# Performance work log

Hardware: AMD Instinct MI355X
Metric: run time of the kernel (lower is better)

Reference implementation:

```python
import jax, jax.numpy as jnp
import numpy as np

NE = 256          # number of electrons
D = 256           # attention_dim = num_heads * heads_dim
H = 4             # num_heads
DH = 64           # heads_dim
L = 2             # num_layers
NDETS = 1
MASK_LEN = 0.1


def _ln(x, s, b):
    m = jnp.mean(x, -1, keepdims=True)
    v = jnp.var(x, -1, keepdims=True)
    return (x - m) * jax.lax.rsqrt(v + 1e-5) * s + b


def setup_inputs() -> dict:
    key = jax.random.key(0)
    ks = jax.random.split(key, 16)
    n = lambda k, sh, sc: (jax.random.normal(k, sh) * sc).astype(jnp.float32)
    theta = jax.random.uniform(ks[0], (NE,), minval=0.1, maxval=np.pi - 0.1)
    phi = jax.random.uniform(ks[1], (NE,), minval=0.0, maxval=2.0 * np.pi)
    return {
        "electrons": jnp.stack([theta, phi], -1).astype(jnp.float32),
        "W_in": n(ks[2], (3, D), 3 ** -0.5),
        "Wq": n(ks[3], (L, D, H, DH), D ** -0.5),
        "bq": jnp.zeros((L, H, DH), jnp.float32),
        "Wk": n(ks[4], (L, D, H, DH), D ** -0.5),
        "bk": jnp.zeros((L, H, DH), jnp.float32),
        "Wv": n(ks[5], (L, D, H, DH), D ** -0.5),
        "bv": jnp.zeros((L, H, DH), jnp.float32),
        "Wo": n(ks[6], (L, H, DH, D), D ** -0.5),
        "bo": jnp.zeros((L, D), jnp.float32),
        "W1": n(ks[7], (L, D, D), D ** -0.5),
        "ln1_s": jnp.ones((L, D), jnp.float32),
        "ln1_b": jnp.zeros((L, D), jnp.float32),
        "W2": n(ks[8], (L, D, D), D ** -0.5),
        "b2": jnp.zeros((L, D), jnp.float32),
        "ln2_s": jnp.ones((L, D), jnp.float32),
        "ln2_b": jnp.zeros((L, D), jnp.float32),
        "Worb_r": n(ks[9], (D, NDETS * 2), D ** -0.5),
        "Worb_i": n(ks[10], (D, NDETS * 2), D ** -0.5),
    }


def reference(electrons, W_in, Wq, bq, Wk, bk, Wv, bv, Wo, bo, W1, ln1_s, ln1_b,
              W2, b2, ln2_s, ln2_b, Worb_r, Worb_i):
    theta, phi = electrons[..., 0], electrons[..., 1]
    # ---- pair gather: P = NE*(NE-1)/2 unordered pairs ----
    iu, ju = jnp.triu_indices(NE, k=1)
    th_p = jnp.stack([theta[iu], theta[ju]], -1)   # [P, 2]
    ph_p = jnp.stack([phi[iu], phi[ju]], -1)       # [P, 2]
    # input_feature: (cos t, sin t cos p, sin t sin p)
    feat = jnp.stack([jnp.cos(th_p), jnp.sin(th_p) * jnp.cos(ph_p),
                      jnp.sin(th_p) * jnp.sin(ph_p)], -1)  # [P, 2, 3]
    # ---- batched mini-transformer over all pairs (seq len 2) ----
    h = feat @ W_in  # [P, 2, D]
    for l in range(L):
        q = jnp.einsum('psd,dhk->pshk', h, Wq[l]) + bq[l]
        k = jnp.einsum('psd,dhk->pshk', h, Wk[l]) + bk[l]
        v = jnp.einsum('psd,dhk->pshk', h, Wv[l]) + bv[l]
        logits = jnp.einsum('pshk,pthk->phst', q / np.sqrt(DH), k)
        attn = jax.nn.softmax(logits, axis=-1)
        o = jnp.einsum('phst,pthk->pshk', attn, v)
        mha = jnp.einsum('pshk,hkd->psd', o, Wo[l]) + bo[l]
        h = h + mha @ W1[l]
        h = _ln(h, ln1_s[l], ln1_b[l])
        h = h + jnp.tanh(h @ W2[l] + b2[l])
        h = _ln(h, ln2_s[l], ln2_b[l])
    # ---- pair orbitals: complex dense -> [P, ndets, 2 elec, 2 orb] ----
    orb = (h @ Worb_r + 1j * (h @ Worb_i)).astype(jnp.complex64)  # [P, 2, ndets*2]
    orb = orb.reshape(-1, 2, NDETS, 2).transpose(0, 2, 1, 3)      # [P, ndets, 2, 2]
    # ---- pairwise truncation factor ----
    u = jnp.cos(th_p / 2) * jnp.exp(1j * ph_p / 2)   # [P, 2]
    v_ = jnp.sin(th_p / 2) * jnp.exp(-1j * ph_p / 2)
    chord = jnp.abs(u[:, 0] * v_[:, 1] - u[:, 1] * v_[:, 0])
    trunc = 1.0 - jnp.exp(-(chord / MASK_LEN) ** 2)  # [P]
    orb = orb * trunc[:, None, None, None]
    dets = jnp.linalg.det(orb)          # [P, ndets]
    pair_orbs = jnp.sum(dets, axis=-1)  # [P]
    # ---- scatter into antisymmetric NE x NE matrix ----
    pf = jnp.zeros((NE, NE), jnp.complex64).at[iu, ju].set(pair_orbs)
    pf = pf - pf.T
    # ---- cusp matrix ----
    ue = jnp.cos(theta / 2) * jnp.exp(0.5j * phi)   # [NE]
    ve = jnp.sin(theta / 2) * jnp.exp(-0.5j * phi)
    elem = ue[:, None] * ve[None, :] - ve[:, None] * ue[None, :]  # [NE, NE]
    eye = jnp.eye(NE, dtype=jnp.float32)
    elem_c = elem + eye
    rho_c = jnp.abs(elem_c)
    cusp = elem_c * jnp.exp(-(rho_c / MASK_LEN) ** 2)
    # ---- pfaffian = sqrt(det), in log space for stability ----
    sign, logabs = jnp.linalg.slogdet(pf + cusp)
    log_ferm = 0.5 * (logabs.astype(jnp.complex64) + 1j * jnp.angle(sign))
    # ---- bosonic flux attachment (truncated product), in log space ----
    rho = jnp.abs(elem)
    masked = jnp.sqrt(MASK_LEN ** 2 + rho ** 2) * elem / (rho + eye) + eye
    log_bos = jnp.sum(jnp.log(masked.astype(jnp.complex64)))
    return log_ferm + log_bos
```

## Files before the change

### kernel.cpp

```cpp
#include <hip/hip_runtime.h>
#include <math.h>
#include <stdint.h>

#define NE 256
#define DD 256
#define NL 2
#define P_TOT 32640
#define NB 32
#define NBP 40
#define NPANEL (NE / NB)
#define NXCD 8

typedef __bf16 bf16x8 __attribute__((ext_vector_type(8)));
typedef float f32x4 __attribute__((ext_vector_type(4)));

__device__ __forceinline__ float bf2f(ushort h) {
    union { unsigned u; float f; } c; c.u = ((unsigned)h) << 16; return c.f;
}
__device__ __forceinline__ ushort f2bf(float f) {
    union { float f; unsigned u; } c; c.f = f;
    unsigned u = c.u;
    return (ushort)((u + 0x7fffu + ((u >> 16) & 1u)) >> 16);
}

#define GLD16(gp, lp) __builtin_amdgcn_global_load_lds( \
    (const __attribute__((address_space(1))) unsigned int*)(uintptr_t)(gp), \
    (__attribute__((address_space(3))) unsigned int*)(uintptr_t)(lp), 16, 0, 0)

__global__ void idx_k(int* __restrict__ ip, int* __restrict__ jp) {
    int i = threadIdx.x;
    int base = i * 255 - (i * (i - 1)) / 2;
    for (int j = i + 1; j < NE; ++j) {
        ip[base + j - i - 1] = i;
        jp[base + j - i - 1] = j;
    }
}

__global__ void zero_k(float* __restrict__ acc) {
    if (threadIdx.x < 8) acc[threadIdx.x] = 0.f;
}

__global__ __launch_bounds__(256) void prep_w_k(
    const float* __restrict__ Wq, const float* __restrict__ Wk, const float* __restrict__ Wv,
    const float* __restrict__ Wo, const float* __restrict__ W1, const float* __restrict__ W2,
    ushort* __restrict__ Wqkv_t, ushort* __restrict__ Woth_t) {
    __shared__ float Ts[32][33];
    int z = blockIdx.z, l = z / 6, m = z % 6;
    const float* src;
    ushort* dst;
    if (m == 0)      { src = Wq + l * 65536; dst = Wqkv_t + (size_t)l * 768 * 256 + 0 * 65536; }
    else if (m == 1) { src = Wk + l * 65536; dst = Wqkv_t + (size_t)l * 768 * 256 + 1 * 65536; }
    else if (m == 2) { src = Wv + l * 65536; dst = Wqkv_t + (size_t)l * 768 * 256 + 2 * 65536; }
    else             { src = (m == 3 ? Wo : m == 4 ? W1 : W2) + l * 65536;
                       dst = Woth_t + (size_t)(l * 3 + (m - 3)) * 65536; }
    int k0 = blockIdx.x * 32, n0 = blockIdx.y * 32;
    int t = threadIdx.x, tr = t >> 5, tc = t & 31;
    for (int i = tr; i < 32; i += 8) Ts[i][tc] = src[(size_t)(k0 + i) * 256 + n0 + tc];
    __syncthreads();
    for (int i = tr; i < 32; i += 8) dst[(size_t)(n0 + i) * 256 + k0 + tc] = f2bf(Ts[tc][i]);
}

__global__ void prep_b_k(const float* __restrict__ bq, const float* __restrict__ bk,
                         const float* __restrict__ bv, float* __restrict__ bqkv) {
    int l = blockIdx.x, t = threadIdx.x;
    bqkv[l * 768 + t] = bq[l * 256 + t];
    bqkv[l * 768 + 256 + t] = bk[l * 256 + t];
    bqkv[l * 768 + 512 + t] = bv[l * 256 + t];
}

__global__ __launch_bounds__(256) void fuse_w_k(
    const float* __restrict__ Wo, const float* __restrict__ W1,
    ushort* __restrict__ Wf_t) {
    __shared__ float WoS[32][33];
    __shared__ float W1S[32][33];
    int l = blockIdx.z;
    int n0 = blockIdx.x * 32, d0 = blockIdx.y * 32;
    const float* wo = Wo + l * 65536;
    const float* w1 = W1 + l * 65536;
    int t = threadIdx.x, ty = t >> 5, tx = t & 31;
    float acc4[4] = {0.f, 0.f, 0.f, 0.f};
    for (int m0 = 0; m0 < 256; m0 += 32) {
        __syncthreads();
        for (int i = ty; i < 32; i += 8) {
            WoS[i][tx] = wo[(size_t)(d0 + i) * 256 + m0 + tx];
            W1S[i][tx] = w1[(size_t)(m0 + i) * 256 + n0 + tx];
        }
        __syncthreads();
#pragma unroll
        for (int jm = 0; jm < 32; ++jm) {
            float a = WoS[tx][jm];
#pragma unroll
            for (int q = 0; q < 4; ++q)
                acc4[q] += a * W1S[jm][ty + 8 * q];
        }
    }
#pragma unroll
    for (int q = 0; q < 4; ++q)
        Wf_t[(size_t)l * 65536 + (size_t)(n0 + ty + 8 * q) * 256 + d0 + tx] = f2bf(acc4[q]);
}

__global__ void fuse_b_k(const float* __restrict__ bo, const float* __restrict__ W1,
                         float* __restrict__ bfuse) {
    int l = blockIdx.x, n = threadIdx.x;
    const float* w1 = W1 + l * 65536;
    const float* b = bo + l * 256;
    float s = 0.f;
    for (int m = 0; m < 256; ++m) s += b[m] * w1[(size_t)m * 256 + n];
    bfuse[l * 256 + n] = s;
}

__global__ __launch_bounds__(256) void embed_k(
    const float* __restrict__ el, const float* __restrict__ Win,
    const int* __restrict__ ip, const int* __restrict__ jp,
    ushort* __restrict__ h, int P0) {
    int w = threadIdx.x >> 6, lane = threadIdx.x & 63;
    int r = blockIdx.x * 4 + w;
    int gp = P0 + (r >> 1);
    int e = (r & 1) ? jp[gp] : ip[gp];
    float th = el[2 * e], ph = el[2 * e + 1];
    float st = sinf(th);
    float f0 = cosf(th), f1 = st * cosf(ph), f2 = st * sinf(ph);
    int n = lane * 4;
    float4 w0 = *(const float4*)&Win[n];
    float4 w1 = *(const float4*)&Win[256 + n];
    float4 w2 = *(const float4*)&Win[512 + n];
    ushort4 o;
    o.x = f2bf(f0 * w0.x + f1 * w1.x + f2 * w2.x);
    o.y = f2bf(f0 * w0.y + f1 * w1.y + f2 * w2.y);
    o.z = f2bf(f0 * w0.z + f1 * w1.z + f2 * w2.z);
    o.w = f2bf(f0 * w0.w + f1 * w1.w + f2 * w2.w);
    *(ushort4*)&h[(size_t)r * 256 + n] = o;
}

template <bool BIAS, bool RES>
__global__ __launch_bounds__(256) void gemm_k(
    const ushort* __restrict__ A, int lda,
    const ushort* __restrict__ Bt,
    const float* __restrict__ bias,
    const ushort* __restrict__ Rm, int ldr,
    ushort* __restrict__ C, int ldc, int ny) {
    __shared__ ushort As[128 * 64];
    __shared__ ushort Bs[128 * 64];
    int t = threadIdx.x, lane = t & 63, w = t >> 6;
    int nwg = gridDim.x;
    int orig = blockIdx.x;
    int qq = nwg / NXCD, rr = nwg % NXCD;
    int xcd = orig % NXCD, idx = orig / NXCD;
    int wg = (xcd < rr ? xcd * (qq + 1) : rr * (qq + 1) + (xcd - rr) * qq) + idx;
    int row0 = (wg / ny) * 128, col0 = (wg % ny) * 128;
    int lrow = lane >> 3;
    int kx = ((lane & 7) ^ lrow) << 3;
    const ushort* gA = A + (size_t)(row0 + w * 32 + lrow) * lda + kx;
    const ushort* gB = Bt + (size_t)(col0 + w * 32 + lrow) * 256 + kx;
    f32x4 acc[4][4];
#pragma unroll
    for (int i = 0; i < 4; ++i)
#pragma unroll
        for (int j = 0; j < 4; ++j) acc[i][j] = (f32x4){0.f, 0.f, 0.f, 0.f};
    int wm = w >> 1, wn = w & 1;
    int mbase = wm * 64 + (lane & 15);
    int nbase = wn * 64 + (lane & 15);
    int l7 = lane & 7;
    for (int k0 = 0; k0 < 256; k0 += 64) {
        __syncthreads();
#pragma unroll
        for (int c2 = 0; c2 < 4; ++c2) {
            GLD16(gA + (size_t)(c2 * 8) * lda + k0, &As[(w * 4 + c2) * 512]);
            GLD16(gB + (size_t)(c2 * 8) * 256 + k0, &Bs[(w * 4 + c2) * 512]);
        }
        __syncthreads();
#pragma unroll
        for (int ks = 0; ks < 2; ++ks) {
            int kb = ks * 4 + (lane >> 4);
            bf16x8 af[4], bfr[4];
#pragma unroll
            for (int tm = 0; tm < 4; ++tm)
                af[tm] = *(const bf16x8*)&As[(mbase + tm * 16) * 64 + ((kb ^ l7) << 3)];
#pragma unroll
            for (int tn = 0; tn < 4; ++tn)
                bfr[tn] = *(const bf16x8*)&Bs[(nbase + tn * 16) * 64 + ((kb ^ l7) << 3)];
#pragma unroll
            for (int tm = 0; tm < 4; ++tm)
#pragma unroll
                for (int tn = 0; tn < 4; ++tn)
                    acc[tm][tn] = __builtin_amdgcn_mfma_f32_16x16x32_bf16(
                        af[tm], bfr[tn], acc[tm][tn], 0, 0, 0);
        }
    }
    int q = lane >> 4;
    int crow = row0 + wm * 64 + q * 4;
    int ccol = col0 + wn * 64 + (lane & 15);
#pragma unroll
    for (int tm = 0; tm < 4; ++tm)
#pragma unroll
        for (int r = 0; r < 4; ++r) {
            int row = crow + tm * 16 + r;
#pragma unroll
            for (int tn = 0; tn < 4; ++tn) {
                int col = ccol + tn * 16;
                float v = acc[tm][tn][r];
                if (BIAS) v += bias[col];
                if (RES) v += bf2f(Rm[(size_t)row * ldr + col]);
                C[(size_t)row * ldc + col] = f2bf(v);
            }
        }
}

template <bool TANH>
__global__ __launch_bounds__(512) void gemm_ln_k(
    const ushort* __restrict__ A, int lda,
    const ushort* __restrict__ Bt,
    const float* __restrict__ bias,
    const ushort* __restrict__ Rm,
    const float* __restrict__ sc, const float* __restrict__ bi,
    ushort* __restrict__ C) {
    __shared__ ushort As[128 * 64];
    __shared__ ushort Bs[256 * 64];
    __shared__ float red_s[128][4][2];
    int t = threadIdx.x, lane = t & 63, w = t >> 6;
    int row0 = blockIdx.x * 128;
    int lrow = lane >> 3;
    int kx = ((lane & 7) ^ lrow) << 3;
    const ushort* gA = A + (size_t)(row0 + w * 16 + lrow) * lda + kx;
    const ushort* gB = Bt + (size_t)(w * 32 + lrow) * 256 + kx;
    f32x4 acc[4][4];
#pragma unroll
    for (int i = 0; i < 4; ++i)
#pragma unroll
        for (int j = 0; j < 4; ++j) acc[i][j] = (f32x4){0.f, 0.f, 0.f, 0.f};
    int wm = w >> 2, wn = w & 3;
    int mbase = wm * 64 + (lane & 15);
    int nbase = wn * 64 + (lane & 15);
    int l7 = lane & 7;
    for (int k0 = 0; k0 < 256; k0 += 64) {
        __syncthreads();
#pragma unroll
        for (int c2 = 0; c2 < 2; ++c2)
            GLD16(gA + (size_t)(c2 * 8) * lda + k0, &As[(w * 2 + c2) * 512]);
#pragma unroll
        for (int c2 = 0; c2 < 4; ++c2)
            GLD16(gB + (size_t)(c2 * 8) * 256 + k0, &Bs[(w * 4 + c2) * 512]);
        __syncthreads();
#pragma unroll
        for (int ks = 0; ks < 2; ++ks) {
            int kb = ks * 4 + (lane >> 4);
            bf16x8 af[4], bfr[4];
#pragma unroll
            for (int tm = 0; tm < 4; ++tm)
                af[tm] = *(const bf16x8*)&As[(mbase + tm * 16) * 64 + ((kb ^ l7) << 3)];
#pragma unroll
            for (int tn = 0; tn < 4; ++tn)
                bfr[tn] = *(const bf16x8*)&Bs[(nbase + tn * 16) * 64 + ((kb ^ l7) << 3)];
#pragma unroll
            for (int tm = 0; tm < 4; ++tm)
#pragma unroll
                for (int tn = 0; tn < 4; ++tn)
                    acc[tm][tn] = __builtin_amdgcn_mfma_f32_16x16x32_bf16(
                        af[tm], bfr[tn], acc[tm][tn], 0, 0, 0);
        }
    }
    int q = lane >> 4;
    float bias4[4];
#pragma unroll
    for (int tn = 0; tn < 4; ++tn) bias4[tn] = bias[wn * 64 + (lane & 15) + tn * 16];
#pragma unroll
    for (int tm = 0; tm < 4; ++tm)
#pragma unroll
        for (int r = 0; r < 4; ++r) {
            int rl = wm * 64 + tm * 16 + q * 4 + r;
            int row = row0 + rl;
            float s = 0.f, sq = 0.f;
#pragma unroll
            for (int tn = 0; tn < 4; ++tn) {
                int col = wn * 64 + (lane & 15) + tn * 16;
                float v = acc[tm][tn][r] + bias4[tn];
                float x;
                if (TANH) x = bf2f(Rm[(size_t)row * 256 + col]) + tanhf(v);
                else      x = v + bf2f(Rm[(size_t)row * 256 + col]);
                acc[tm][tn][r] = x;
                s += x; sq += x * x;
            }
#pragma unroll
            for (int off = 1; off <= 8; off <<= 1) {
                s += __shfl_xor(s, off, 64);
                sq += __shfl_xor(sq, off, 64);
            }
            if ((lane & 15) == 0) { red_s[rl][wn][0] = s; red_s[rl][wn][1] = sq; }
        }
    __syncthreads();
    float sc4[4], bi4[4];
#pragma unroll
    for (int tn = 0; tn < 4; ++tn) {
        int col = wn * 64 + (lane & 15) + tn * 16;
        sc4[tn] = sc[col]; bi4[tn] = bi[col];
    }
#pragma unroll
    for (int tm = 0; tm < 4; ++tm)
#pragma unroll
        for (int r = 0; r < 4; ++r) {
            int rl = wm * 64 + tm * 16 + q * 4 + r;
            int row = row0 + rl;
            float m = (red_s[rl][0][0] + red_s[rl][1][0] +
                       red_s[rl][2][0] + red_s[rl][3][0]) * (1.f / 256.f);
            float var = (red_s[rl][0][1] + red_s[rl][1][1] +
                         red_s[rl][2][1] + red_s[rl][3][1]) * (1.f / 256.f) - m * m;
            float rs = rsqrtf(var + 1e-5f);
#pragma unroll
            for (int tn = 0; tn < 4; ++tn) {
                int col = wn * 64 + (lane & 15) + tn * 16;
                C[(size_t)row * 256 + col] =
                    f2bf((acc[tm][tn][r] - m) * rs * sc4[tn] + bi4[tn]);
            }
        }
}

__global__ __launch_bounds__(256) void attn_k(ushort* __restrict__ qkv) {
    int wid = threadIdx.x >> 6, lane = threadIdx.x & 63;
    int gw = blockIdx.x * 4 + wid;
    int p = gw >> 2, hh = gw & 3;
    size_t r0 = (size_t)(2 * p) * 768 + hh * 64 + lane;
    size_t r1 = r0 + 768;
    float q0 = bf2f(qkv[r0]) * 0.125f, q1 = bf2f(qkv[r1]) * 0.125f;
    float k0 = bf2f(qkv[r0 + 256]), k1 = bf2f(qkv[r1 + 256]);
    float v0 = bf2f(qkv[r0 + 512]), v1 = bf2f(qkv[r1 + 512]);
    float s00 = q0 * k0, s01 = q0 * k1, s10 = q1 * k0, s11 = q1 * k1;
#pragma unroll
    for (int off = 32; off; off >>= 1) {
        s00 += __shfl_xor(s00, off, 64);
        s01 += __shfl_xor(s01, off, 64);
        s10 += __shfl_xor(s10, off, 64);
        s11 += __shfl_xor(s11, off, 64);
    }
    float m0 = fmaxf(s00, s01), m1 = fmaxf(s10, s11);
    float e00 = expf(s00 - m0), e01 = expf(s01 - m0);
    float e10 = expf(s10 - m1), e11 = expf(s11 - m1);
    float i0 = 1.f / (e00 + e01), i1 = 1.f / (e10 + e11);
    float o0 = (e00 * i0) * v0 + (e01 * i0) * v1;
    float o1 = (e10 * i1) * v0 + (e11 * i1) * v1;
    qkv[r0] = f2bf(o0);
    qkv[r1] = f2bf(o1);
}

__global__ __launch_bounds__(256) void orb_k(
    const ushort* __restrict__ h, const float* __restrict__ Wr, const float* __restrict__ Wi,
    const float* __restrict__ el, const int* __restrict__ ip, const int* __restrict__ jp,
    float2* __restrict__ porb, int P0) {
    int w = threadIdx.x >> 6, lane = threadIdx.x & 63;
    int p = blockIdx.x * 4 + w;
    const ushort* h0 = h + (size_t)(2 * p) * 256;
    int d0 = lane * 4;
    ushort4 a0 = *(const ushort4*)&h0[d0];
    ushort4 a1 = *(const ushort4*)&h0[256 + d0];
    float x0[4] = {bf2f(a0.x), bf2f(a0.y), bf2f(a0.z), bf2f(a0.w)};
    float x1[4] = {bf2f(a1.x), bf2f(a1.y), bf2f(a1.z), bf2f(a1.w)};
    float wrv[8], wiv[8];
    *(float4*)&wrv[0] = *(const float4*)&Wr[2 * d0];
    *(float4*)&wrv[4] = *(const float4*)&Wr[2 * d0 + 4];
    *(float4*)&wiv[0] = *(const float4*)&Wi[2 * d0];
    *(float4*)&wiv[4] = *(const float4*)&Wi[2 * d0 + 4];
    float s[8] = {0, 0, 0, 0, 0, 0, 0, 0};
#pragma unroll
    for (int u = 0; u < 4; ++u) {
        s[0] += x0[u] * wrv[2 * u];     s[1] += x0[u] * wiv[2 * u];
        s[2] += x0[u] * wrv[2 * u + 1]; s[3] += x0[u] * wiv[2 * u + 1];
        s[4] += x1[u] * wrv[2 * u];     s[5] += x1[u] * wiv[2 * u];
        s[6] += x1[u] * wrv[2 * u + 1]; s[7] += x1[u] * wiv[2 * u + 1];
    }
#pragma unroll
    for (int off = 32; off; off >>= 1) {
#pragma unroll
        for (int q2 = 0; q2 < 8; ++q2) s[q2] += __shfl_xor(s[q2], off, 64);
    }
    if (lane == 0) {
        int gp = P0 + p;
        int i = ip[gp], j = jp[gp];
        float thi = el[2 * i], phi_ = el[2 * i + 1];
        float thj = el[2 * j], phj = el[2 * j + 1];
        float chi = cosf(thi * 0.5f), shi = sinf(thi * 0.5f);
        float chj = cosf(thj * 0.5f), shj = sinf(thj * 0.5f);
        float cpi = cosf(phi_ * 0.5f), spi = sinf(phi_ * 0.5f);
        float cpj = cosf(phj * 0.5f), spj = sinf(phj * 0.5f);
        float uix = chi * cpi, uiy = chi * spi;
        float vix = shi * cpi, viy = -shi * spi;
        float ujx = chj * cpj, ujy = chj * spj;
        float vjx = shj * cpj, vjy = -shj * spj;
        float crx = (uix * vjx - uiy * vjy) - (ujx * vix - ujy * viy);
        float cry = (uix * vjy + uiy * vjx) - (ujx * viy + ujy * vix);
        float chord2 = crx * crx + cry * cry;
        float trunc = 1.f - expf(-100.f * chord2);
        float t2 = trunc * trunc;
        float dr = (s[0] * s[6] - s[1] * s[7]) - (s[2] * s[4] - s[3] * s[5]);
        float di = (s[0] * s[7] + s[1] * s[6]) - (s[2] * s[5] + s[3] * s[4]);
        porb[gp] = make_float2(dr * t2, di * t2);
    }
}

__global__ __launch_bounds__(256) void assemble_k(
    const float* __restrict__ el, const float2* __restrict__ porb,
    float2* __restrict__ Am, float* acc) {
    __shared__ float sre[256], sim[256];
    int idx = blockIdx.x * 256 + threadIdx.x;
    int i = idx >> 8, j = idx & 255;
    float thi = el[2 * i], phi_ = el[2 * i + 1];
    float thj = el[2 * j], phj = el[2 * j + 1];
    float chi = cosf(thi * 0.5f), shi = sinf(thi * 0.5f);
    float chj = cosf(thj * 0.5f), shj = sinf(thj * 0.5f);
    float cpi = cosf(phi_ * 0.5f), spi = sinf(phi_ * 0.5f);
    float cpj = cosf(phj * 0.5f), spj = sinf(phj * 0.5f);
    float uix = chi * cpi, uiy = chi * spi;
    float vix = shi * cpi, viy = -shi * spi;
    float ujx = chj * cpj, ujy = chj * spj;
    float vjx = shj * cpj, vjy = -shj * spj;
    float ex = (uix * vjx - uiy * vjy) - (ujx * vix - ujy * viy);
    float ey = (uix * vjy + uiy * vjx) - (ujx * viy + ujy * vix);
    float pfx = 0.f, pfy = 0.f;
    if (i < j) {
        int pp = i * 255 - (i * (i - 1)) / 2 + (j - i - 1);
        float2 t = porb[pp]; pfx = t.x; pfy = t.y;
    } else if (i > j) {
        int pp = j * 255 - (j * (j - 1)) / 2 + (i - j - 1);
        float2 t = porb[pp]; pfx = -t.x; pfy = -t.y;
    }
    float eye = (i == j) ? 1.f : 0.f;
    float ecx = ex + eye, ecy = ey;
    float wgt = expf(-100.f * (ecx * ecx + ecy * ecy));
    Am[idx] = make_float2(pfx + ecx * wgt, pfy + ecy * wgt);
    float lre = 0.f, lim = 0.f;
    if (i != j) {
        float r2 = ex * ex + ey * ey;
        lre = 0.5f * logf(0.01f + r2);
        lim = atan2f(ey, ex);
    }
    sre[threadIdx.x] = lre; sim[threadIdx.x] = lim;
    __syncthreads();
    for (int s2 = 128; s2; s2 >>= 1) {
        if (threadIdx.x < s2) {
            sre[threadIdx.x] += sre[threadIdx.x + s2];
            sim[threadIdx.x] += sim[threadIdx.x + s2];
        }
        __syncthreads();
    }
    if (threadIdx.x == 0) {
        atomicAdd(acc + 0, sre[0]);
        atomicAdd(acc + 1, sim[0]);
    }
}

__device__ __forceinline__ unsigned wave_max_u32_dpp(unsigned m) {
#define DPP_STEP(ctrl) { \
    unsigned tmp_ = (unsigned)__builtin_amdgcn_update_dpp((int)m, (int)m, ctrl, 0xf, 0xf, false); \
    m = (m >= tmp_) ? m : tmp_; }
    DPP_STEP(0x111)
    DPP_STEP(0x112)
    DPP_STEP(0x114)
    DPP_STEP(0x118)
    DPP_STEP(0x142)
    DPP_STEP(0x143)
#undef DPP_STEP
    return (unsigned)__builtin_amdgcn_readlane((int)m, 63);
}

__global__ __launch_bounds__(256) void panel_k(
    float2* __restrict__ Am, float* __restrict__ acc, int k0) {
    __shared__ float2 Pn[NBP][NE];
    __shared__ alignas(16) unsigned rbest4[2][4];
    __shared__ float2 diag_s[NB];
    __shared__ short piv_s[NB];
    __shared__ short phys_of_s[NB];
    __shared__ float2 Ls[NB][NB + 1];
    __shared__ short sigma_s[NE];
    __shared__ short rlist_s[NB];
    __shared__ int rcount_s;
    int t = threadIdx.x, lane = t & 63, w = t >> 6;
    int nr = NE - k0;
    bool act = t < nr;
    float2 cur = make_float2(0.f, 0.f);
    if (act) {
        const float4* src = (const float4*)(Am + (size_t)(k0 + t) * NE + k0);
#pragma unroll
        for (int c2 = 0; c2 < NB / 2; ++c2) {
            float4 v = src[c2];
            Pn[2 * c2][t]     = make_float2(v.x, v.y);
            Pn[2 * c2 + 1][t] = make_float2(v.z, v.w);
            if (c2 == 0) cur = make_float2(v.x, v.y);
        }
    }
    __syncthreads();
    int lg = t;
    int nsw = 0;
#pragma unroll 1
    for (int j = 0; j < NB; ++j) {
        const int par = j & 1;
        unsigned pk = 0u;
        if (act && lg >= j) {
            float fv = fabsf(cur.x) + fabsf(cur.y);
            union { float f; unsigned u; } cu; cu.f = fv;
            pk = (cu.u & 0xFFFF0000u) | ((unsigned)lg << 8) | (unsigned)t;
        }
        unsigned wbest = wave_max_u32_dpp(pk);
        if (lane == 0) rbest4[par][w] = wbest;
        __syncthreads();
        uint4 rb = *(const uint4*)&rbest4[par][0];
        unsigned ga = rb.x >= rb.y ? rb.x : rb.y;
        unsigned gb = rb.z >= rb.w ? rb.z : rb.w;
        unsigned gg = ga >= gb ? ga : gb;
        int w_phys = (int)(gg & 255u);
        int l_w    = (int)((gg >> 8) & 255u);
        float2 d = Pn[j][w_phys];
        if (t == 0) {
            diag_s[j] = d;
            piv_s[j] = (short)l_w;
            if (l_w != j) nsw++;
        }
        int oldlg = lg;
        if (t == w_phys) lg = j;
        else if (oldlg == j) lg = l_w;
        float ivn = 1.f / (d.x * d.x + d.y * d.y);
        float inx = d.x * ivn, iny = -d.y * ivn;
        if (act && lg > j) {
            float2 L = make_float2(cur.x * inx - cur.y * iny,
                                   cur.x * iny + cur.y * inx);
            Pn[j][t] = L;
            if (j < NB - 1) {
                float2 u1 = Pn[j + 1][w_phys];
                float2 v1 = Pn[j + 1][t];
                v1.x -= L.x * u1.x - L.y * u1.y;
                v1.y -= L.x * u1.y + L.y * u1.x;
                Pn[j + 1][t] = v1;
                cur = v1;
                int nch = (NB - 2 - j + 7) >> 3;
#pragma unroll 1
                for (int ch = 0; ch < nch; ++ch) {
                    int c0 = j + 2 + ch * 8;
                    const float2* ub = &Pn[c0][w_phys];
                    float2* vb = &Pn[c0][t];
                    float2 uu[8], vv[8];
#pragma unroll
                    for (int cc = 0; cc < 8; ++cc) uu[cc] = ub[(size_t)cc * NE];
#pragma unroll
                    for (int cc = 0; cc < 8; ++cc) vv[cc] = vb[(size_t)cc * NE];
#pragma unroll
                    for (int cc = 0; cc < 8; ++cc) {
                        vv[cc].x -= L.x * uu[cc].x - L.y * uu[cc].y;
                        vv[cc].y -= L.x * uu[cc].y + L.y * uu[cc].x;
                    }
#pragma unroll
                    for (int cc = 0; cc < 8; ++cc) vb[(size_t)cc * NE] = vv[cc];
                }
            }
        }
    }
    if (act && lg < NB) phys_of_s[lg] = (short)t;
    if (act) {
        float4* dst = (float4*)(Am + (size_t)(k0 + lg) * NE + k0);
#pragma unroll
        for (int c2 = 0; c2 < NB / 2; ++c2) {
            float2 e0 = Pn[2 * c2][t], e1 = Pn[2 * c2 + 1][t];
            dst[c2] = make_float4(e0.x, e0.y, e1.x, e1.y);
        }
    }
    __syncthreads();
    if (w == 0) {
        float lre = 0.f, lim = 0.f;
        if (lane < NB) {
            float2 d = diag_s[lane];
            lre = 0.5f * logf(d.x * d.x + d.y * d.y);
            lim = atan2f(d.y, d.x);
        }
#pragma unroll
        for (int off = 32; off; off >>= 1) {
            lre += __shfl_xor(lre, off, 64);
            lim += __shfl_xor(lim, off, 64);
        }
        if (lane == 0) { acc[2] += lre; acc[3] += lim; }
    }
    if (t == 0) acc[4] += (float)nsw;
    if (k0 + NB >= NE) return;
    for (int idx = t; idx < NB * NB; idx += 256) {
        int i2 = idx >> 5, j2 = idx & 31;
        Ls[i2][j2] = Pn[j2][phys_of_s[i2]];
    }
    sigma_s[t] = (short)t;
    if (t < NB) rlist_s[t] = (short)k0;
    __syncthreads();
    if (t == 0) {
        for (int j2 = 0; j2 < NB; ++j2) {
            int p = k0 + (int)piv_s[j2], r1 = k0 + j2;
            short tmp = sigma_s[r1]; sigma_s[r1] = sigma_s[p]; sigma_s[p] = tmp;
        }
        int cnt = 0;
        for (int r2 = k0 + NB; r2 < NE; ++r2)
            if (sigma_s[r2] != r2) rlist_s[cnt++] = (short)r2;
        rcount_s = cnt;
    }
    __syncthreads();
    int ncols = NE - k0 - NB;
    if (t >= ncols) return;
    int col = k0 + NB + t;
    int cnt = rcount_s;
    float2 x[NB];
#pragma unroll
    for (int i = 0; i < NB; ++i)
        x[i] = Am[(size_t)sigma_s[k0 + i] * NE + col];
    float2 extra[NB];
#pragma unroll
    for (int q2 = 0; q2 < NB; ++q2)
        extra[q2] = Am[(size_t)sigma_s[rlist_s[q2]] * NE + col];
#pragma unroll
    for (int i = 1; i < NB; ++i) {
        float2 xi = x[i];
#pragma unroll
        for (int j2 = 0; j2 < i; ++j2) {
            float2 l = Ls[i][j2];
            xi.x -= l.x * x[j2].x - l.y * x[j2].y;
            xi.y -= l.x * x[j2].y + l.y * x[j2].x;
        }
        x[i] = xi;
    }
#pragma unroll
    for (int i = 0; i < NB; ++i)
        Am[(size_t)(k0 + i) * NE + col] = x[i];
#pragma unroll
    for (int q2 = 0; q2 < NB; ++q2)
        if (q2 < cnt) Am[(size_t)rlist_s[q2] * NE + col] = extra[q2];
}

__global__ __launch_bounds__(256) void update_k(float2* __restrict__ Am, int k0) {
    __shared__ float2 Lt[NB][NB + 1];
    __shared__ float2 Ut[NB][NB + 1];
    int t = threadIdx.x;
    int r0 = k0 + NB + blockIdx.x * NB;
    int c0 = k0 + NB + blockIdx.y * NB;
    for (int idx = t; idx < NB * NB; idx += 256) {
        int a = idx >> 5, b = idx & 31;
        Lt[a][b] = Am[(size_t)(r0 + a) * NE + k0 + b];
        Ut[a][b] = Am[(size_t)(k0 + a) * NE + c0 + b];
    }
    __syncthreads();
    int lr = t >> 3, lc0 = (t & 7) * 4;
    float2 s0 = {0.f, 0.f}, s1 = {0.f, 0.f}, s2 = {0.f, 0.f}, s3 = {0.f, 0.f};
#pragma unroll
    for (int k = 0; k < NB; ++k) {
        float2 a = Lt[lr][k];
        float2 u0 = Ut[k][lc0 + 0], u1 = Ut[k][lc0 + 1];
        float2 u2 = Ut[k][lc0 + 2], u3 = Ut[k][lc0 + 3];
        s0.x += a.x * u0.x - a.y * u0.y; s0.y += a.x * u0.y + a.y * u0.x;
        s1.x += a.x * u1.x - a.y * u1.y; s1.y += a.x * u1.y + a.y * u1.x;
        s2.x += a.x * u2.x - a.y * u2.y; s2.y += a.x * u2.y + a.y * u2.x;
        s3.x += a.x * u3.x - a.y * u3.y; s3.y += a.x * u3.y + a.y * u3.x;
    }
    size_t base = (size_t)(r0 + lr) * NE + c0 + lc0;
    float2 cc;
    cc = Am[base + 0]; cc.x -= s0.x; cc.y -= s0.y; Am[base + 0] = cc;
    cc = Am[base + 1]; cc.x -= s1.x; cc.y -= s1.y; Am[base + 1] = cc;
    cc = Am[base + 2]; cc.x -= s2.x; cc.y -= s2.y; Am[base + 2] = cc;
    cc = Am[base + 3]; cc.x -= s3.x; cc.y -= s3.y; Am[base + 3] = cc;
}

__global__ void finalize_k(const float* __restrict__ acc, float* __restrict__ out) {
    if (threadIdx.x == 0) {
        float ang = acc[3] + 3.14159265358979323846f * acc[4];
        ang -= 6.283185307179586f * rintf(ang * 0.15915494309189535f);
        out[0] = 0.5f * acc[2] + acc[0];
        out[1] = 0.5f * ang + acc[1];
    }
}

extern "C" void kernel_launch(void* const* d_in, const int* in_sizes, int n_in,
                              void* d_out, int out_size, void* d_ws, size_t ws_size,
                              hipStream_t stream) {
    (void)in_sizes; (void)n_in; (void)out_size;
    const float* el   = (const float*)d_in[0];
    const float* Win  = (const float*)d_in[1];
    const float* Wq   = (const float*)d_in[2];
    const float* bq   = (const float*)d_in[3];
    const float* Wk   = (const float*)d_in[4];
    const float* bk   = (const float*)d_in[5];
    const float* Wv   = (const float*)d_in[6];
    const float* bv   = (const float*)d_in[7];
    const float* Wo   = (const float*)d_in[8];
    const float* bo   = (const float*)d_in[9];
    const float* W1   = (const float*)d_in[10];
    const float* ln1s = (const float*)d_in[11];
    const float* ln1b = (const float*)d_in[12];
    const float* W2   = (const float*)d_in[13];
    const float* b2   = (const float*)d_in[14];
    const float* ln2s = (const float*)d_in[15];
    const float* ln2b = (const float*)d_in[16];
    const float* Wor  = (const float*)d_in[17];
    const float* Woi  = (const float*)d_in[18];

    char* wp = (char*)d_ws;
    auto alloc = [&](size_t b) {
        char* r = wp;
        wp += (b + 255) & ~(size_t)255;
        return r;
    };
    int*    ipb  = (int*)alloc((size_t)P_TOT * 4);
    int*    jpb  = (int*)alloc((size_t)P_TOT * 4);
    float2* porb = (float2*)alloc((size_t)P_TOT * 8);
    float2* Am   = (float2*)alloc((size_t)NE * NE * 8);
    float*  acc  = (float*)alloc(256);
    ushort* Wqkv_t = (ushort*)alloc((size_t)2 * 768 * 256 * 2);
    ushort* Woth_t = (ushort*)alloc((size_t)6 * 65536 * 2);
    ushort* Wf_t   = (ushort*)alloc((size_t)2 * 65536 * 2);
    float*  bfuse  = (float*)alloc((size_t)2 * 256 * 4);
    float*  bqkv = (float*)alloc((size_t)2 * 768 * 4);
    size_t fixed = (size_t)(wp - (char*)d_ws);

    int nchunk = 0, PCr = 0, MCr = 0;
    const int cands[3] = {1, 2, 3};
    for (int ci = 0; ci < 3; ++ci) {
        int pc = P_TOT / cands[ci];
        size_t mc = (size_t)2 * pc;
        size_t var = 0;
        var += ((mc * 256 * 2 + 255) & ~(size_t)255);
        var += ((mc * 768 * 2 + 255) & ~(size_t)255);
        if (fixed + var <= ws_size) { nchunk = cands[ci]; PCr = pc; MCr = (int)mc; break; }
    }
    if (!nchunk) {
        zero_k<<<1, 64, 0, stream>>>((float*)d_out);
        return;
    }
    ushort* hb   = (ushort*)alloc((size_t)MCr * 256 * 2);
    ushort* qkvb = (ushort*)alloc((size_t)MCr * 768 * 2);
    int MTr = MCr / 128;

    prep_w_k<<<dim3(8, 8, 12), 256, 0, stream>>>(Wq, Wk, Wv, Wo, W1, W2, Wqkv_t, Woth_t);
    prep_b_k<<<2, 256, 0, stream>>>(bq, bk, bv, bqkv);
    fuse_w_k<<<dim3(8, 8, 2), 256, 0, stream>>>(Wo, W1, Wf_t);
    fuse_b_k<<<2, 256, 0, stream>>>(bo, W1, bfuse);
    idx_k<<<1, 256, 0, stream>>>(ipb, jpb);
    zero_k<<<1, 64, 0, stream>>>(acc);

    for (int c = 0; c < nchunk; ++c) {
        int P0 = c * PCr;
        embed_k<<<MCr / 4, 256, 0, stream>>>(el, Win, ipb, jpb, hb, P0);
        for (int l = 0; l < NL; ++l) {
            gemm_k<true, false><<<MTr * 6, 256, 0, stream>>>(
                hb, 256, Wqkv_t + (size_t)l * 768 * 256, bqkv + l * 768, nullptr, 0, qkvb, 768, 6);
            attn_k<<<PCr, 256, 0, stream>>>(qkvb);
            gemm_ln_k<false><<<MTr, 512, 0, stream>>>(
                qkvb, 768, Wf_t + (size_t)l * 65536, bfuse + l * 256, hb,
                ln1s + l * 256, ln1b + l * 256, hb);
            gemm_ln_k<true><<<MTr, 512, 0, stream>>>(
                hb, 256, Woth_t + (size_t)(l * 3 + 2) * 65536, b2 + l * 256, hb,
                ln2s + l * 256, ln2b + l * 256, hb);
        }
        orb_k<<<PCr / 4, 256, 0, stream>>>(hb, Wor, Woi, el, ipb, jpb, porb, P0);
    }
    assemble_k<<<NE, 256, 0, stream>>>(el, porb, Am, acc);

    for (int p = 0; p < NPANEL; ++p) {
        int k0 = p * NB;
        panel_k<<<1, 256, 0, stream>>>(Am, acc, k0);
        int m = NE - k0 - NB;
        if (m > 0) {
            dim3 ug(m / NB, m / NB);
            update_k<<<ug, 256, 0, stream>>>(Am, k0);
        }
    }
    finalize_k<<<1, 64, 0, stream>>>(acc, (float*)d_out);
}
```

Measured before the change: 943.1 us.

## Publish pivot row values with argmax and software-pipeline panel column updates

In the LU panel kernel, the winning thread of each wave now publishes its current, next and next-next column values together with the packed pivot key in shared memory. This removes the dependent shared-memory reads of the pivot row after the barrier. The two leading trailing columns are kept in registers (cur/nxt), and the remaining column chunks are software-pipelined so the next chunk's loads are issued before the current chunk is computed and stored. The price is more registers and a more complex swap/writeback path for the pivot row.

```diff
diff --git a/kernel.cpp b/kernel.cpp
--- a/kernel.cpp
+++ b/kernel.cpp
@@ -463,7 +463,7 @@
 __global__ __launch_bounds__(256) void panel_k(
     float2* __restrict__ Am, float* __restrict__ acc, int k0) {
     __shared__ float2 Pn[NBP][NE];
-    __shared__ alignas(16) unsigned rbest4[2][4];
+    __shared__ alignas(16) float pub[2][4][8];
     __shared__ float2 diag_s[NB];
     __shared__ short piv_s[NB];
     __shared__ short phys_of_s[NB];
@@ -475,6 +475,7 @@
     int nr = NE - k0;
     bool act = t < nr;
     float2 cur = make_float2(0.f, 0.f);
+    float2 nxt = make_float2(0.f, 0.f);
     if (act) {
         const float4* src = (const float4*)(Am + (size_t)(k0 + t) * NE + k0);
 #pragma unroll
@@ -482,7 +483,7 @@
             float4 v = src[c2];
             Pn[2 * c2][t]     = make_float2(v.x, v.y);
             Pn[2 * c2 + 1][t] = make_float2(v.z, v.w);
-            if (c2 == 0) cur = make_float2(v.x, v.y);
+            if (c2 == 0) { cur = make_float2(v.x, v.y); nxt = make_float2(v.z, v.w); }
         }
     }
     __syncthreads();
@@ -497,24 +498,48 @@
             union { float f; unsigned u; } cu; cu.f = fv;
             pk = (cu.u & 0xFFFF0000u) | ((unsigned)lg << 8) | (unsigned)t;
         }
+        float2 own2 = make_float2(0.f, 0.f);
+        if (act && j + 2 < NB) own2 = Pn[j + 2][t];
         unsigned wbest = wave_max_u32_dpp(pk);
-        if (lane == 0) rbest4[par][w] = wbest;
+        if (lane == 0) pub[par][w][0] = __uint_as_float(wbest);
+        if (pk != 0u && pk == wbest) {
+            pub[par][w][2] = cur.x;  pub[par][w][3] = cur.y;
+            pub[par][w][4] = nxt.x;  pub[par][w][5] = nxt.y;
+            pub[par][w][6] = own2.x; pub[par][w][7] = own2.y;
+        }
         __syncthreads();
-        uint4 rb = *(const uint4*)&rbest4[par][0];
-        unsigned ga = rb.x >= rb.y ? rb.x : rb.y;
-        unsigned gb = rb.z >= rb.w ? rb.z : rb.w;
-        unsigned gg = ga >= gb ? ga : gb;
+        float4 s0a = *(const float4*)&pub[par][0][0];
+        float4 s0b = *(const float4*)&pub[par][0][4];
+        float4 s1a = *(const float4*)&pub[par][1][0];
+        float4 s1b = *(const float4*)&pub[par][1][4];
+        float4 s2a = *(const float4*)&pub[par][2][0];
+        float4 s2b = *(const float4*)&pub[par][2][4];
+        float4 s3a = *(const float4*)&pub[par][3][0];
+        float4 s3b = *(const float4*)&pub[par][3][4];
+        unsigned p0 = __float_as_uint(s0a.x), p1 = __float_as_uint(s1a.x);
+        unsigned p2 = __float_as_uint(s2a.x), p3 = __float_as_uint(s3a.x);
+        unsigned ga; float4 va, vb_;
+        if (p0 >= p1) { ga = p0; va = s0a; vb_ = s0b; } else { ga = p1; va = s1a; vb_ = s1b; }
+        unsigned gb; float4 wa, wb2;
+        if (p2 >= p3) { gb = p2; wa = s2a; wb2 = s2b; } else { gb = p3; wa = s3a; wb2 = s3b; }
+        unsigned gg; float4 xa, xb;
+        if (ga >= gb) { gg = ga; xa = va; xb = vb_; } else { gg = gb; xa = wa; xb = wb2; }
         int w_phys = (int)(gg & 255u);
         int l_w    = (int)((gg >> 8) & 255u);
-        float2 d = Pn[j][w_phys];
+        float2 d  = make_float2(xa.z, xa.w);
+        float2 u1 = make_float2(xb.x, xb.y);
+        float2 u2 = make_float2(xb.z, xb.w);
         if (t == 0) {
             diag_s[j] = d;
             piv_s[j] = (short)l_w;
             if (l_w != j) nsw++;
         }
         int oldlg = lg;
-        if (t == w_phys) lg = j;
-        else if (oldlg == j) lg = l_w;
+        if (t == w_phys) {
+            lg = j;
+            Pn[j][t] = cur;
+            if (j + 1 < NB) Pn[j + 1][t] = nxt;
+        } else if (oldlg == j) lg = l_w;
         float ivn = 1.f / (d.x * d.x + d.y * d.y);
         float inx = d.x * ivn, iny = -d.y * ivn;
         if (act && lg > j) {
@@ -522,30 +547,57 @@
                                    cur.x * iny + cur.y * inx);
             Pn[j][t] = L;
             if (j < NB - 1) {
-                float2 u1 = Pn[j + 1][w_phys];
-                float2 v1 = Pn[j + 1][t];
-                v1.x -= L.x * u1.x - L.y * u1.y;
-                v1.y -= L.x * u1.y + L.y * u1.x;
-                Pn[j + 1][t] = v1;
-                cur = v1;
-                int nch = (NB - 2 - j + 7) >> 3;
+                cur.x = nxt.x - (L.x * u1.x - L.y * u1.y);
+                cur.y = nxt.y - (L.x * u1.y + L.y * u1.x);
+                if (j + 2 < NB) {
+                    nxt.x = own2.x - (L.x * u2.x - L.y * u2.y);
+                    nxt.y = own2.y - (L.x * u2.y + L.y * u2.x);
+                }
+                int c = j + 3;
+                if (c < NB) {
+                    float2 uA[8], vA[8];
+                    {
+                        const float2* ub = &Pn[c][w_phys];
+                        float2* vb = &Pn[c][t];
+#pragma unroll
+                        for (int cc = 0; cc < 8; ++cc) {
+                            uA[cc] = ub[(size_t)cc * NE];
+                            vA[cc] = vb[(size_t)cc * NE];
+                        }
+                    }
+                    int cA = c;
+                    c += 8;
 #pragma unroll 1
-                for (int ch = 0; ch < nch; ++ch) {
-                    int c0 = j + 2 + ch * 8;
-                    const float2* ub = &Pn[c0][w_phys];
-                    float2* vb = &Pn[c0][t];
-                    float2 uu[8], vv[8];
-#pragma unroll
-                    for (int cc = 0; cc < 8; ++cc) uu[cc] = ub[(size_t)cc * NE];
-#pragma unroll
-                    for (int cc = 0; cc < 8; ++cc) vv[cc] = vb[(size_t)cc * NE];
+                    while (c < NB) {
+                        float2 uB[8], vB[8];
+                        {
+                            const float2* ub = &Pn[c][w_phys];
+                            float2* vb = &Pn[c][t];
+#pragma unroll
+                            for (int cc = 0; cc < 8; ++cc) {
+                                uB[cc] = ub[(size_t)cc * NE];
+                                vB[cc] = vb[(size_t)cc * NE];
+                            }
+                        }
+                        float2* vo = &Pn[cA][t];
+#pragma unroll
+                        for (int cc = 0; cc < 8; ++cc) {
+                            vA[cc].x -= L.x * uA[cc].x - L.y * uA[cc].y;
+                            vA[cc].y -= L.x * uA[cc].y + L.y * uA[cc].x;
+                            vo[(size_t)cc * NE] = vA[cc];
+                        }
+#pragma unroll
+                        for (int cc = 0; cc < 8; ++cc) { uA[cc] = uB[cc]; vA[cc] = vB[cc]; }
+                        cA = c;
+                        c += 8;
+                    }
+                    float2* vo = &Pn[cA][t];
 #pragma unroll
                     for (int cc = 0; cc < 8; ++cc) {
-                        vv[cc].x -= L.x * uu[cc].x - L.y * uu[cc].y;
-                        vv[cc].y -= L.x * uu[cc].y + L.y * uu[cc].x;
+                        vA[cc].x -= L.x * uA[cc].x - L.y * uA[cc].y;
+                        vA[cc].y -= L.x * uA[cc].y + L.y * uA[cc].x;
+                        vo[(size_t)cc * NE] = vA[cc];
                     }
-#pragma unroll
-                    for (int cc = 0; cc < 8; ++cc) vb[(size_t)cc * NE] = vv[cc];
                 }
             }
         }
```

Result: slower. 998.4 us (+5.9%).
